# Kernel optimization log

Measured on AMD Instinct MI355X. Metric: run time of the kernel, lower is better.

Reference implementation:

```python
import jax, jax.numpy as jnp
import numpy as np

N_NODES = 100000
EPS = 1e-5


def _layernorm(x, g, b):
    # per-node layer norm over feature dim
    mu = jnp.mean(x, axis=-1, keepdims=True)
    var = jnp.mean(jnp.square(x - mu), axis=-1, keepdims=True)
    return (x - mu) * jax.lax.rsqrt(var + EPS) * g + b


def _gcn_conv(x, W, b, src, dst, n_nodes):
    # GCNConv: xW, then symmetric-normalized aggregation with self-loops.
    xw = x @ W  # [N, out]
    ones = jnp.ones(src.shape[0], dtype=x.dtype)
    deg = jax.ops.segment_sum(ones, dst, num_segments=n_nodes) + 1.0  # +1 self loop
    dinv = jax.lax.rsqrt(deg)  # [N]
    norm = dinv[src] * dinv[dst]  # [E]
    msg = xw[src] * norm[:, None]  # [E, out]  <- dominant memory traffic
    agg = jax.ops.segment_sum(msg, dst, num_segments=n_nodes)
    agg = agg + xw * (dinv * dinv)[:, None]  # self-loop contribution
    return agg + b


def setup_inputs() -> dict:
    key = jax.random.key(0)
    ks = jax.random.split(key, 16)
    in_c, hid, out_c = 128, 64, 32
    E = 1_600_000
    d = {}
    d['x'] = jax.random.normal(ks[0], (N_NODES, in_c), dtype=jnp.float32)
    d['edge_index'] = jax.random.randint(ks[1], (2, E), 0, N_NODES, dtype=jnp.int64)

    def lin(k, fi, fo):
        s = 1.0 / np.sqrt(fi)
        k1, k2 = jax.random.split(k)
        return (jax.random.uniform(k1, (fi, fo), jnp.float32, -s, s),
                jax.random.uniform(k2, (fo,), jnp.float32, -s, s))

    d['W1'], d['b1'] = lin(ks[2], in_c, hid)
    d['g1'], d['be1'] = jnp.ones((hid,), jnp.float32), jnp.zeros((hid,), jnp.float32)
    d['W2'], d['b2'] = lin(ks[3], hid, 2 * hid)
    d['g2'], d['be2'] = jnp.ones((2 * hid,), jnp.float32), jnp.zeros((2 * hid,), jnp.float32)
    d['W3'], d['b3'] = lin(ks[4], 2 * hid, hid)
    d['g3'], d['be3'] = jnp.ones((hid,), jnp.float32), jnp.zeros((hid,), jnp.float32)
    d['lw1'], d['lb1'] = lin(ks[5], hid, hid // 2)
    d['g4'], d['be4'] = jnp.ones((hid // 2,), jnp.float32), jnp.zeros((hid // 2,), jnp.float32)
    d['lw2'], d['lb2'] = lin(ks[6], hid // 2, out_c)
    return d


def reference(x, edge_index, W1, b1, g1, be1, W2, b2, g2, be2, W3, b3, g3, be3,
              lw1, lb1, g4, be4, lw2, lb2):
    src, dst = edge_index[0], edge_index[1]
    h = _gcn_conv(x, W1, b1, src, dst, N_NODES)
    h = jax.nn.elu(_layernorm(h, g1, be1))
    h = _gcn_conv(h, W2, b2, src, dst, N_NODES)
    h = jax.nn.elu(_layernorm(h, g2, be2))
    h = _gcn_conv(h, W3, b3, src, dst, N_NODES)
    h = jax.nn.elu(_layernorm(h, g3, be3))
    h = h @ lw1 + lb1
    h = jax.nn.elu(_layernorm(h, g4, be4))
    return h @ lw2 + lb2
```

## Files before the change

### kernel.cpp

```cpp
#include <hip/hip_runtime.h>
#include <math.h>

#define N_NODES 100000
#define LN_EPS 1e-5f
#define NBUCK ((N_NODES + 255) / 256)
#define EPB 8192

typedef __attribute__((ext_vector_type(8))) short bf16x8;
typedef __attribute__((ext_vector_type(4))) float f32x4;

__device__ __forceinline__ unsigned short f2bf(float f) {
    unsigned int u = __float_as_uint(f);
    return (unsigned short)((u + 0x7FFFu + ((u >> 16) & 1u)) >> 16);
}
__device__ __forceinline__ float bf2f(unsigned short u) {
    return __uint_as_float(((unsigned int)u) << 16);
}


__global__ void count_edges(const int* __restrict__ dst, int* __restrict__ counts, int E) {
    __shared__ int hist[NBUCK];
    for (int b = threadIdx.x; b < NBUCK; b += 512) hist[b] = 0;
    __syncthreads();
    int e0 = blockIdx.x * EPB;
#pragma unroll 4
    for (int i = 0; i < EPB / 512; ++i) {
        int e = e0 + i * 512 + (int)threadIdx.x;
        if (e < E) atomicAdd(&hist[((unsigned)dst[e]) >> 8], 1);
    }
    __syncthreads();
    for (int b = threadIdx.x; b < NBUCK; b += 512)
        counts[blockIdx.x * NBUCK + b] = hist[b];
}

__global__ void scan_pos(const int* __restrict__ counts, int* __restrict__ pos,
                         int* __restrict__ tot, int nblk) {
    __shared__ int s[512];
    int b = blockIdx.x, i = threadIdx.x;
    int v = (i < nblk) ? counts[i * NBUCK + b] : 0;
    s[i] = v;
    __syncthreads();
    for (int off = 1; off < 512; off <<= 1) {
        int t = (i >= off) ? s[i - off] : 0;
        __syncthreads();
        s[i] += t;
        __syncthreads();
    }
    if (i < nblk) pos[i * NBUCK + b] = s[i] - v;
    if (i == 511) tot[b] = s[511];
}

__global__ void scan_base(const int* __restrict__ tot, int* __restrict__ base, int E) {
    __shared__ int s[512];
    int i = threadIdx.x;
    int v = (i < NBUCK) ? tot[i] : 0;
    s[i] = v;
    __syncthreads();
    for (int off = 1; off < 512; off <<= 1) {
        int t = (i >= off) ? s[i - off] : 0;
        __syncthreads();
        s[i] += t;
        __syncthreads();
    }
    if (i < NBUCK) base[i] = s[i] - v;
    if (i == 0) base[NBUCK] = E;
}

__global__ void place_edges(const int* __restrict__ src, const int* __restrict__ dst,
                            const int* __restrict__ pos, const int* __restrict__ base,
                            unsigned* __restrict__ bucket, int E) {
    __shared__ int lcur[NBUCK];
    for (int b = threadIdx.x; b < NBUCK; b += 512)
        lcur[b] = pos[blockIdx.x * NBUCK + b] + base[b];
    __syncthreads();
    int e0 = blockIdx.x * EPB;
#pragma unroll 4
    for (int i = 0; i < EPB / 512; ++i) {
        int e = e0 + i * 512 + (int)threadIdx.x;
        if (e < E) {
            unsigned d = (unsigned)dst[e];
            unsigned s = (unsigned)src[e];
            int p = atomicAdd(&lcur[d >> 8], 1);
            bucket[p] = ((d & 255u) << 24) | s;
        }
    }
}

__global__ void build_csr_node(const unsigned* __restrict__ bucket, const int* __restrict__ base,
                               int* __restrict__ offsets, float* __restrict__ dinv,
                               int* __restrict__ csr, int E) {
    __shared__ int hist[256];
    __shared__ int cur[256];
    int b = blockIdx.x, t = threadIdx.x;
    int r0 = b << 8;
    hist[t] = 0;
    __syncthreads();
    int s0 = base[b], s1 = base[b + 1];
    for (int e = s0 + t; e < s1; e += 256)
        atomicAdd(&hist[bucket[e] >> 24], 1);
    __syncthreads();
    int deg = hist[t];
    for (int off = 1; off < 256; off <<= 1) {
        int tv = (t >= off) ? hist[t - off] : 0;
        __syncthreads();
        hist[t] += tv;
        __syncthreads();
    }
    int excl = hist[t] - deg;
    int node = r0 + t;
    if (node < N_NODES) {
        offsets[node] = s0 + excl;
        dinv[node] = rsqrtf((float)deg + 1.f);
        cur[t] = s0 + excl;
    }
    if (node == N_NODES - 1) offsets[N_NODES] = E;
    __syncthreads();
    for (int e = s0 + t; e < s1; e += 256) {
        unsigned u = bucket[e];
        int p = atomicAdd(&cur[u >> 24], 1);
        csr[p] = (int)(u & 0xFFFFFFu);
    }
}

template <int K, int OUT, bool LN, bool BIAS, bool AF32, bool OF32>
__launch_bounds__(256)
__global__ void mfma_gemm(const void* __restrict__ Xv, const float* __restrict__ W,
                          const float* __restrict__ bias, const float* __restrict__ gamma,
                          const float* __restrict__ beta, void* __restrict__ Yv, int n) {
    constexpr int T  = OUT / 16;
    constexpr int KP = K + 8;

    __shared__ __align__(16) unsigned short sWT[OUT * KP];
    for (int i = threadIdx.x; i < K * OUT; i += 256) {
        int k = i / OUT, o = i - k * OUT;
        sWT[o * KP + k] = f2bf(W[i]);
    }
    __syncthreads();

    int wv = threadIdx.x >> 6, lane = threadIdx.x & 63;
    int quad = lane >> 4, l16 = lane & 15;
    int m0 = (blockIdx.x * 4 + wv) * 16;
    int rowc = min(m0 + l16, n - 1);

    f32x4 acc[T];
#pragma unroll
    for (int t = 0; t < T; ++t) acc[t] = (f32x4){0.f, 0.f, 0.f, 0.f};

#pragma unroll
    for (int s = 0; s < K / 32; ++s) {
        int koff = s * 32 + quad * 8;
        bf16x8 af;
        if (AF32) {
            const float4* X4 = (const float4*)Xv;
            size_t base = ((size_t)rowc * K + koff) >> 2;
            float4 a0 = X4[base];
            float4 a1 = X4[base + 1];
            af[0] = (short)f2bf(a0.x); af[1] = (short)f2bf(a0.y);
            af[2] = (short)f2bf(a0.z); af[3] = (short)f2bf(a0.w);
            af[4] = (short)f2bf(a1.x); af[5] = (short)f2bf(a1.y);
            af[6] = (short)f2bf(a1.z); af[7] = (short)f2bf(a1.w);
        } else {
            const unsigned short* Xb = (const unsigned short*)Xv;
            af = *(const bf16x8*)(Xb + (size_t)rowc * K + koff);
        }
#pragma unroll
        for (int t = 0; t < T; ++t) {
            const bf16x8 bfrag = *(const bf16x8*)&sWT[(t * 16 + l16) * KP + koff];
            acc[t] = __builtin_amdgcn_mfma_f32_16x16x32_bf16(af, bfrag, acc[t], 0, 0, 0);
        }
    }

    float bj[T], gj[T], btj[T];
#pragma unroll
    for (int t = 0; t < T; ++t) {
        int c = t * 16 + l16;
        bj[t]  = BIAS ? bias[c] : 0.f;
        gj[t]  = LN ? gamma[c] : 1.f;
        btj[t] = LN ? beta[c] : 0.f;
    }

    float* Yf = (float*)Yv;
    unsigned short* Yb = (unsigned short*)Yv;

    if (LN) {
        float s[4] = {0.f, 0.f, 0.f, 0.f}, sq[4] = {0.f, 0.f, 0.f, 0.f};
#pragma unroll
        for (int t = 0; t < T; ++t)
#pragma unroll
            for (int r = 0; r < 4; ++r) {
                float v = acc[t][r] + bj[t];
                s[r] += v;
                sq[r] += v * v;
            }
#pragma unroll
        for (int off = 1; off < 16; off <<= 1)
#pragma unroll
            for (int r = 0; r < 4; ++r) {
                s[r] += __shfl_xor(s[r], off, 64);
                sq[r] += __shfl_xor(sq[r], off, 64);
            }
        float mu[4], rs[4];
#pragma unroll
        for (int r = 0; r < 4; ++r) {
            mu[r] = s[r] / OUT;
            float var = sq[r] / OUT - mu[r] * mu[r];
            rs[r] = rsqrtf(var + LN_EPS);
        }
#pragma unroll
        for (int r = 0; r < 4; ++r) {
            int rowg = m0 + quad * 4 + r;
            if (rowg < n) {
#pragma unroll
                for (int t = 0; t < T; ++t) {
                    float y = (acc[t][r] + bj[t] - mu[r]) * rs[r] * gj[t] + btj[t];
                    y = y > 0.f ? y : expm1f(y);
                    size_t idx = (size_t)rowg * OUT + t * 16 + l16;
                    if (OF32) Yf[idx] = y; else Yb[idx] = f2bf(y);
                }
            }
        }
    } else {
#pragma unroll
        for (int r = 0; r < 4; ++r) {
            int rowg = m0 + quad * 4 + r;
            if (rowg < n) {
#pragma unroll
                for (int t = 0; t < T; ++t) {
                    float y = acc[t][r] + bj[t];
                    size_t idx = (size_t)rowg * OUT + t * 16 + l16;
                    if (OF32) Yf[idx] = y; else Yb[idx] = f2bf(y);
                }
            }
        }
    }
}

template <bool LN>
__global__ void gather64(const unsigned short* __restrict__ xw, const int* __restrict__ offsets,
                         const int* __restrict__ csr_src, const float* __restrict__ dinv,
                         const float* __restrict__ bias, const float* __restrict__ gamma,
                         const float* __restrict__ beta, unsigned short* __restrict__ out, int n) {
    int wave = threadIdx.x >> 6;
    int lane = threadIdx.x & 63;
    int node = blockIdx.x * (blockDim.x >> 6) + wave;
    if (node >= n) return;
    int beg = offsets[node], end = offsets[node + 1];
    int quad = lane >> 4, q16 = lane & 15;
    int c0 = q16 * 4;

    float a0 = 0.f, a1 = 0.f, a2 = 0.f, a3 = 0.f;
    for (int base = beg; base < end; base += 64) {
        int m = min(64, end - base);
        int myS = (lane < m) ? csr_src[base + lane] : 0;
        float myN = (lane < m) ? dinv[myS] : 0.f;
#pragma unroll 4
        for (int j4 = 0; j4 < m; j4 += 4) {
            int e = j4 + quad;
            int s = __shfl(myS, e, 64);
            float nm = __shfl(myN, e, 64);
            ushort4 r = *(const ushort4*)(xw + (size_t)s * 64 + c0);
            a0 += bf2f(r.x) * nm;
            a1 += bf2f(r.y) * nm;
            a2 += bf2f(r.z) * nm;
            a3 += bf2f(r.w) * nm;
        }
    }
    a0 += __shfl_xor(a0, 16, 64); a0 += __shfl_xor(a0, 32, 64);
    a1 += __shfl_xor(a1, 16, 64); a1 += __shfl_xor(a1, 32, 64);
    a2 += __shfl_xor(a2, 16, 64); a2 += __shfl_xor(a2, 32, 64);
    a3 += __shfl_xor(a3, 16, 64); a3 += __shfl_xor(a3, 32, 64);

    float dd = dinv[node];
    ushort4 sr = *(const ushort4*)(xw + (size_t)node * 64 + c0);
    float y0 = a0 * dd + bf2f(sr.x) * dd * dd;
    float y1 = a1 * dd + bf2f(sr.y) * dd * dd;
    float y2 = a2 * dd + bf2f(sr.z) * dd * dd;
    float y3 = a3 * dd + bf2f(sr.w) * dd * dd;

    if (!LN) {
        if (quad == 0) {
            ushort4 o;
            o.x = f2bf(y0); o.y = f2bf(y1); o.z = f2bf(y2); o.w = f2bf(y3);
            *(ushort4*)(out + (size_t)node * 64 + c0) = o;
        }
        return;
    }
    float4 bv = *(const float4*)(bias + c0);
    float4 gv = *(const float4*)(gamma + c0);
    float4 tv = *(const float4*)(beta + c0);
    y0 += bv.x; y1 += bv.y; y2 += bv.z; y3 += bv.w;
    float s = y0 + y1 + y2 + y3;
    float sq = y0 * y0 + y1 * y1 + y2 * y2 + y3 * y3;
#pragma unroll
    for (int off = 1; off < 16; off <<= 1) {
        s += __shfl_xor(s, off, 64);
        sq += __shfl_xor(sq, off, 64);
    }
    float mu = s / 64.f;
    float var = sq / 64.f - mu * mu;
    float rs = rsqrtf(var + LN_EPS);
    float z0 = (y0 - mu) * rs * gv.x + tv.x; z0 = z0 > 0.f ? z0 : expm1f(z0);
    float z1 = (y1 - mu) * rs * gv.y + tv.y; z1 = z1 > 0.f ? z1 : expm1f(z1);
    float z2 = (y2 - mu) * rs * gv.z + tv.z; z2 = z2 > 0.f ? z2 : expm1f(z2);
    float z3 = (y3 - mu) * rs * gv.w + tv.w; z3 = z3 > 0.f ? z3 : expm1f(z3);
    if (quad == 0) {
        ushort4 o;
        o.x = f2bf(z0); o.y = f2bf(z1); o.z = f2bf(z2); o.w = f2bf(z3);
        *(ushort4*)(out + (size_t)node * 64 + c0) = o;
    }
}

extern "C" void kernel_launch(void* const* d_in, const int* in_sizes, int n_in,
                              void* d_out, int out_size, void* d_ws, size_t ws_size,
                              hipStream_t stream) {
    const float* x  = (const float*)d_in[0];
    const int* ei   = (const int*)d_in[1];
    const float* W1 = (const float*)d_in[2];
    const float* b1 = (const float*)d_in[3];
    const float* g1 = (const float*)d_in[4];
    const float* be1= (const float*)d_in[5];
    const float* W2 = (const float*)d_in[6];
    const float* b2 = (const float*)d_in[7];
    const float* g2 = (const float*)d_in[8];
    const float* be2= (const float*)d_in[9];
    const float* W3 = (const float*)d_in[10];
    const float* b3 = (const float*)d_in[11];
    const float* g3 = (const float*)d_in[12];
    const float* be3= (const float*)d_in[13];
    const float* lw1= (const float*)d_in[14];
    const float* lb1= (const float*)d_in[15];
    const float* g4 = (const float*)d_in[16];
    const float* be4= (const float*)d_in[17];
    const float* lw2= (const float*)d_in[18];
    const float* lb2= (const float*)d_in[19];
    float* out = (float*)d_out;

    const int E = in_sizes[1] / 2;
    const int* src = ei;
    const int* dst = ei + E;
    const int N = N_NODES;

    unsigned short* bufA = (unsigned short*)d_ws;
    unsigned short* bufB = bufA + (size_t)N * 128;
    float* dinv    = (float*)(bufB + (size_t)N * 128);
    int*   offsets = (int*)(dinv + N);
    int*   csr     = offsets + N + 1;
    int*   tot     = csr + E;
    int*   base    = tot + NBUCK;

    auto cdiv = [](long long a, long long b) { return (int)((a + b - 1) / b); };
    const int NBLK = cdiv(E, EPB);

    int* counts = (int*)bufA;
    int* pos    = counts + (size_t)NBLK * NBUCK;
    unsigned* bucket = (unsigned*)bufB;

    const int NB = cdiv(N, 256);
    const int GB = cdiv(N, 64);
    (void)NB;

    count_edges<<<NBLK, 512, 0, stream>>>(dst, counts, E);
    scan_pos<<<NBUCK, 512, 0, stream>>>(counts, pos, tot, NBLK);
    scan_base<<<1, 512, 0, stream>>>(tot, base, E);
    place_edges<<<NBLK, 512, 0, stream>>>(src, dst, pos, base, bucket, E);
    build_csr_node<<<NBUCK, 256, 0, stream>>>(bucket, base, offsets, dinv, csr, E);

    mfma_gemm<128, 64, false, false, true, false><<<GB, 256, 0, stream>>>(
        x, W1, nullptr, nullptr, nullptr, bufA, N);
    gather64<true><<<cdiv(N, 4), 256, 0, stream>>>(bufA, offsets, csr, dinv, b1, g1, be1, bufB, N);

    gather64<false><<<cdiv(N, 4), 256, 0, stream>>>(bufB, offsets, csr, dinv, nullptr, nullptr, nullptr, bufA, N);
    mfma_gemm<64, 128, true, true, false, false><<<GB, 256, 0, stream>>>(
        bufA, W2, b2, g2, be2, bufB, N);

    mfma_gemm<128, 64, false, false, false, false><<<GB, 256, 0, stream>>>(
        bufB, W3, nullptr, nullptr, nullptr, bufA, N);
    gather64<true><<<cdiv(N, 4), 256, 0, stream>>>(bufA, offsets, csr, dinv, b3, g3, be3, bufB, N);

    mfma_gemm<64, 32, true, true, false, false><<<GB, 256, 0, stream>>>(
        bufB, lw1, lb1, g4, be4, bufA, N);

    mfma_gemm<32, 32, false, true, false, true><<<GB, 256, 0, stream>>>(
        bufA, lw2, lb2, nullptr, nullptr, out, N);
}
```

Measured before the change: 389.4 us.

## Fold source-side degree scaling into producers and gather full rows per edge

Each producer of a gathered feature matrix (GEMM epilogue or previous gather) now multiplies its rows by dinv, so the aggregation no longer needs a per-edge dinv lookup and multiply. Only the destination scale is applied at the end, and the self-loop term becomes part of the same sum. The gather also changes layout: each wave reads a whole 64-feature row per edge, one bf16 element per lane, with source indices broadcast via readlane, instead of four edges per iteration at four features per lane. This drops the cross-quad reduction but issues narrower 2-byte loads per lane. Pre-scaling before the bf16 rounding slightly changes numerics.

```diff
diff --git a/kernel.cpp b/kernel.cpp
--- a/kernel.cpp
+++ b/kernel.cpp
@@ -122,11 +122,12 @@
     }
 }
 
-template <int K, int OUT, bool LN, bool BIAS, bool AF32, bool OF32>
+template <int K, int OUT, bool LN, bool BIAS, bool AF32, bool OF32, bool SCALED>
 __launch_bounds__(256)
 __global__ void mfma_gemm(const void* __restrict__ Xv, const float* __restrict__ W,
                           const float* __restrict__ bias, const float* __restrict__ gamma,
-                          const float* __restrict__ beta, void* __restrict__ Yv, int n) {
+                          const float* __restrict__ beta, void* __restrict__ Yv, int n,
+                          const float* __restrict__ dinvp) {
     constexpr int T  = OUT / 16;
     constexpr int KP = K + 8;
 
@@ -210,10 +211,12 @@
         for (int r = 0; r < 4; ++r) {
             int rowg = m0 + quad * 4 + r;
             if (rowg < n) {
+                float dv = SCALED ? dinvp[rowg] : 1.f;
 #pragma unroll
                 for (int t = 0; t < T; ++t) {
                     float y = (acc[t][r] + bj[t] - mu[r]) * rs[r] * gj[t] + btj[t];
                     y = y > 0.f ? y : expm1f(y);
+                    if (SCALED) y *= dv;
                     size_t idx = (size_t)rowg * OUT + t * 16 + l16;
                     if (OF32) Yf[idx] = y; else Yb[idx] = f2bf(y);
                 }
@@ -224,9 +227,11 @@
         for (int r = 0; r < 4; ++r) {
             int rowg = m0 + quad * 4 + r;
             if (rowg < n) {
+                float dv = SCALED ? dinvp[rowg] : 1.f;
 #pragma unroll
                 for (int t = 0; t < T; ++t) {
                     float y = acc[t][r] + bj[t];
+                    if (SCALED) y *= dv;
                     size_t idx = (size_t)rowg * OUT + t * 16 + l16;
                     if (OF32) Yf[idx] = y; else Yb[idx] = f2bf(y);
                 }
@@ -235,79 +240,64 @@
     }
 }
 
-template <bool LN>
-__global__ void gather64(const unsigned short* __restrict__ xw, const int* __restrict__ offsets,
-                         const int* __restrict__ csr_src, const float* __restrict__ dinv,
-                         const float* __restrict__ bias, const float* __restrict__ gamma,
-                         const float* __restrict__ beta, unsigned short* __restrict__ out, int n) {
+template <bool LN, bool SCALEOUT>
+__global__ void gather_rl(const unsigned short* __restrict__ xs, const int* __restrict__ offsets,
+                          const int* __restrict__ csr_src, const float* __restrict__ dinv,
+                          const float* __restrict__ bias, const float* __restrict__ gamma,
+                          const float* __restrict__ beta, unsigned short* __restrict__ out, int n) {
     int wave = threadIdx.x >> 6;
     int lane = threadIdx.x & 63;
     int node = blockIdx.x * (blockDim.x >> 6) + wave;
     if (node >= n) return;
     int beg = offsets[node], end = offsets[node + 1];
-    int quad = lane >> 4, q16 = lane & 15;
-    int c0 = q16 * 4;
 
     float a0 = 0.f, a1 = 0.f, a2 = 0.f, a3 = 0.f;
     for (int base = beg; base < end; base += 64) {
         int m = min(64, end - base);
         int myS = (lane < m) ? csr_src[base + lane] : 0;
-        float myN = (lane < m) ? dinv[myS] : 0.f;
-#pragma unroll 4
-        for (int j4 = 0; j4 < m; j4 += 4) {
-            int e = j4 + quad;
-            int s = __shfl(myS, e, 64);
-            float nm = __shfl(myN, e, 64);
-            ushort4 r = *(const ushort4*)(xw + (size_t)s * 64 + c0);
-            a0 += bf2f(r.x) * nm;
-            a1 += bf2f(r.y) * nm;
-            a2 += bf2f(r.z) * nm;
-            a3 += bf2f(r.w) * nm;
-        }
-    }
-    a0 += __shfl_xor(a0, 16, 64); a0 += __shfl_xor(a0, 32, 64);
-    a1 += __shfl_xor(a1, 16, 64); a1 += __shfl_xor(a1, 32, 64);
-    a2 += __shfl_xor(a2, 16, 64); a2 += __shfl_xor(a2, 32, 64);
-    a3 += __shfl_xor(a3, 16, 64); a3 += __shfl_xor(a3, 32, 64);
+        int k = 0;
+        for (; k + 4 <= m; k += 4) {
+            int s0 = __builtin_amdgcn_readlane(myS, k);
+            int s1 = __builtin_amdgcn_readlane(myS, k + 1);
+            int s2 = __builtin_amdgcn_readlane(myS, k + 2);
+            int s3 = __builtin_amdgcn_readlane(myS, k + 3);
+            unsigned short v0 = xs[((size_t)s0 << 6) + lane];
+            unsigned short v1 = xs[((size_t)s1 << 6) + lane];
+            unsigned short v2 = xs[((size_t)s2 << 6) + lane];
+            unsigned short v3 = xs[((size_t)s3 << 6) + lane];
+            a0 += bf2f(v0);
+            a1 += bf2f(v1);
+            a2 += bf2f(v2);
+            a3 += bf2f(v3);
+        }
+        for (; k < m; ++k) {
+            int s0 = __builtin_amdgcn_readlane(myS, k);
+            a0 += bf2f(xs[((size_t)s0 << 6) + lane]);
+        }
+    }
 
     float dd = dinv[node];
-    ushort4 sr = *(const ushort4*)(xw + (size_t)node * 64 + c0);
-    float y0 = a0 * dd + bf2f(sr.x) * dd * dd;
-    float y1 = a1 * dd + bf2f(sr.y) * dd * dd;
-    float y2 = a2 * dd + bf2f(sr.z) * dd * dd;
-    float y3 = a3 * dd + bf2f(sr.w) * dd * dd;
+    float self = bf2f(xs[((size_t)node << 6) + lane]);
+    float y = (a0 + a1 + a2 + a3 + self) * dd;
 
     if (!LN) {
-        if (quad == 0) {
-            ushort4 o;
-            o.x = f2bf(y0); o.y = f2bf(y1); o.z = f2bf(y2); o.w = f2bf(y3);
-            *(ushort4*)(out + (size_t)node * 64 + c0) = o;
-        }
+        out[((size_t)node << 6) + lane] = f2bf(y);
         return;
     }
-    float4 bv = *(const float4*)(bias + c0);
-    float4 gv = *(const float4*)(gamma + c0);
-    float4 tv = *(const float4*)(beta + c0);
-    y0 += bv.x; y1 += bv.y; y2 += bv.z; y3 += bv.w;
-    float s = y0 + y1 + y2 + y3;
-    float sq = y0 * y0 + y1 * y1 + y2 * y2 + y3 * y3;
-#pragma unroll
-    for (int off = 1; off < 16; off <<= 1) {
+    float yb = y + bias[lane];
+    float s = yb, sq = yb * yb;
+#pragma unroll
+    for (int off = 1; off < 64; off <<= 1) {
         s += __shfl_xor(s, off, 64);
         sq += __shfl_xor(sq, off, 64);
     }
-    float mu = s / 64.f;
-    float var = sq / 64.f - mu * mu;
+    float mu = s * (1.f / 64.f);
+    float var = sq * (1.f / 64.f) - mu * mu;
     float rs = rsqrtf(var + LN_EPS);
-    float z0 = (y0 - mu) * rs * gv.x + tv.x; z0 = z0 > 0.f ? z0 : expm1f(z0);
-    float z1 = (y1 - mu) * rs * gv.y + tv.y; z1 = z1 > 0.f ? z1 : expm1f(z1);
-    float z2 = (y2 - mu) * rs * gv.z + tv.z; z2 = z2 > 0.f ? z2 : expm1f(z2);
-    float z3 = (y3 - mu) * rs * gv.w + tv.w; z3 = z3 > 0.f ? z3 : expm1f(z3);
-    if (quad == 0) {
-        ushort4 o;
-        o.x = f2bf(z0); o.y = f2bf(z1); o.z = f2bf(z2); o.w = f2bf(z3);
-        *(ushort4*)(out + (size_t)node * 64 + c0) = o;
-    }
+    float z = (yb - mu) * rs * gamma[lane] + beta[lane];
+    z = z > 0.f ? z : expm1f(z);
+    if (SCALEOUT) z *= dd;
+    out[((size_t)node << 6) + lane] = f2bf(z);
 }
 
 extern "C" void kernel_launch(void* const* d_in, const int* in_sizes, int n_in,
@@ -355,9 +345,7 @@
     int* pos    = counts + (size_t)NBLK * NBUCK;
     unsigned* bucket = (unsigned*)bufB;
 
-    const int NB = cdiv(N, 256);
     const int GB = cdiv(N, 64);
-    (void)NB;
 
     count_edges<<<NBLK, 512, 0, stream>>>(dst, counts, E);
     scan_pos<<<NBUCK, 512, 0, stream>>>(counts, pos, tot, NBLK);
@@ -365,21 +353,21 @@
     place_edges<<<NBLK, 512, 0, stream>>>(src, dst, pos, base, bucket, E);
     build_csr_node<<<NBUCK, 256, 0, stream>>>(bucket, base, offsets, dinv, csr, E);
 
-    mfma_gemm<128, 64, false, false, true, false><<<GB, 256, 0, stream>>>(
-        x, W1, nullptr, nullptr, nullptr, bufA, N);
-    gather64<true><<<cdiv(N, 4), 256, 0, stream>>>(bufA, offsets, csr, dinv, b1, g1, be1, bufB, N);
-
-    gather64<false><<<cdiv(N, 4), 256, 0, stream>>>(bufB, offsets, csr, dinv, nullptr, nullptr, nullptr, bufA, N);
-    mfma_gemm<64, 128, true, true, false, false><<<GB, 256, 0, stream>>>(
-        bufA, W2, b2, g2, be2, bufB, N);
-
-    mfma_gemm<128, 64, false, false, false, false><<<GB, 256, 0, stream>>>(
-        bufB, W3, nullptr, nullptr, nullptr, bufA, N);
-    gather64<true><<<cdiv(N, 4), 256, 0, stream>>>(bufA, offsets, csr, dinv, b3, g3, be3, bufB, N);
-
-    mfma_gemm<64, 32, true, true, false, false><<<GB, 256, 0, stream>>>(
-        bufB, lw1, lb1, g4, be4, bufA, N);
-
-    mfma_gemm<32, 32, false, true, false, true><<<GB, 256, 0, stream>>>(
-        bufA, lw2, lb2, nullptr, nullptr, out, N);
-}
+    mfma_gemm<128, 64, false, false, true, false, true><<<GB, 256, 0, stream>>>(
+        x, W1, nullptr, nullptr, nullptr, bufA, N, dinv);
+    gather_rl<true, true><<<cdiv(N, 4), 256, 0, stream>>>(bufA, offsets, csr, dinv, b1, g1, be1, bufB, N);
+
+    gather_rl<false, false><<<cdiv(N, 4), 256, 0, stream>>>(bufB, offsets, csr, dinv, nullptr, nullptr, nullptr, bufA, N);
+    mfma_gemm<64, 128, true, true, false, false, false><<<GB, 256, 0, stream>>>(
+        bufA, W2, b2, g2, be2, bufB, N, nullptr);
+
+    mfma_gemm<128, 64, false, false, false, false, true><<<GB, 256, 0, stream>>>(
+        bufB, W3, nullptr, nullptr, nullptr, bufA, N, dinv);
+    gather_rl<true, false><<<cdiv(N, 4), 256, 0, stream>>>(bufA, offsets, csr, dinv, b3, g3, be3, bufB, N);
+
+    mfma_gemm<64, 32, true, true, false, false, false><<<GB, 256, 0, stream>>>(
+        bufB, lw1, lb1, g4, be4, bufA, N, nullptr);
+
+    mfma_gemm<32, 32, false, true, false, true, false><<<GB, 256, 0, stream>>>(
+        bufA, lw2, lb2, nullptr, nullptr, out, N, nullptr);
+}
```

Measured after the change: 377.4 us. -3.1%, faster.
